# Kernel tuning notes

Hardware: AMD Instinct MI355X
Metric: run time of the kernel (lower is better)

The kernel has to match this reference:

```python
import jax, jax.numpy as jnp
import numpy as np

B, N = 2, 6
H, W = 64, 64            # BEV grid
FH, FW = 32, 88          # camera feature map
DIM, FEAT_DIM = 128, 128
HEADS, DH = 4, 32
QW1, QW2 = 8, 8          # query window
KW1, KW2 = 4, 11         # key/val window
IMG_H, IMG_W = 224, 480
EPS = 1e-5


def _ln(t, g, b):
    m = t.mean(-1, keepdims=True)
    v = ((t - m) ** 2).mean(-1, keepdims=True)
    return (t - m) / jnp.sqrt(v + EPS) * g + b


def _bn_relu_conv(t, g, b, Wc):
    # eval-mode BatchNorm2d (running_mean=0, running_var=1) -> ReLU -> 1x1 conv
    y = jax.nn.relu(t / jnp.sqrt(1.0 + EPS) * g[:, None, None] + b[:, None, None])
    return jnp.einsum('oc,nchw->nohw', Wc, y)


def _normalize(t, axis):
    n = jnp.sqrt(jnp.sum(t * t, axis=axis, keepdims=True))
    return t / jnp.maximum(n, 1e-12)


def _win(t, w1, w2):
    # (..., X*w1, Y*w2, d) -> (..., X, Y, w1, w2, d)
    s = t.shape
    t = t.reshape(*s[:-3], s[-3] // w1, w1, s[-2] // w2, w2, s[-1])
    return jnp.swapaxes(t, -4, -3)


def _unwin(t):
    # (..., X, Y, w1, w2, d) -> (..., X*w1, Y*w2, d)
    s = t.shape
    return jnp.swapaxes(t, -4, -3).reshape(*s[:-5], s[-5] * s[-3], s[-4] * s[-2], s[-1])


def _gridwin(t, w1, w2):
    bb, nn, Ht, Wt, d = t.shape
    t = t.reshape(bb, nn, w1, Ht // w1, w2, Wt // w2, d)
    return t.transpose(0, 1, 3, 5, 2, 4, 6)  # (b, n, X, Y, w1, w2, d)


def _cross_win_attn(qw, kw, vw, ln_g, ln_b, Wqkv, bqkv, Wp, bp, skip):
    b, n, X, Y, w1, w2, d = qw.shape
    f1, f2 = kw.shape[4], kw.shape[5]
    L = X * Y
    q = qw.transpose(0, 2, 3, 1, 4, 5, 6).reshape(b, L, n * w1 * w2, d)
    k = kw.transpose(0, 2, 3, 1, 4, 5, 6).reshape(b, L, n * f1 * f2, d)
    v = vw.transpose(0, 2, 3, 1, 4, 5, 6).reshape(b, L, n * f1 * f2, d)
    q = _ln(q, ln_g[0], ln_b[0]) @ Wqkv[0] + bqkv[0]
    k = _ln(k, ln_g[1], ln_b[1]) @ Wqkv[1] + bqkv[1]
    v = _ln(v, ln_g[2], ln_b[2]) @ Wqkv[2] + bqkv[2]
    split = lambda t: t.reshape(*t.shape[:-1], HEADS, DH)  # head-major channel split
    q, k, v = split(q), split(k), split(v)
    att = jax.nn.softmax(DH ** -0.5 * jnp.einsum('blqhd,blkhd->bhlqk', q, k), axis=-1)
    o = jnp.einsum('bhlqk,blkhd->blqhd', att, v).reshape(b, L, n * w1 * w2, HEADS * DH)
    o = o @ Wp + bp
    o = o.reshape(b, X, Y, n, w1, w2, d).mean(3)  # mean over cameras
    return o + skip


def _forward(x, grid, feature, I_inv, E_inv,
             bn_fl_g, bn_fl_b, W_fl, bn_fp_g, bn_fp_b, W_fp,
             W_bev, b_bev, W_img, W_cam,
             attn_ln_g, attn_ln_b, attn_Wqkv, attn_bqkv, attn_Wp, attn_bp,
             pn_g, pn_b, Wma, bma, Wmb, bmb, post_g, post_b):
    b, n = feature.shape[:2]
    # image plane (buffer)
    xs = jnp.linspace(0.0, 1.0, FW) * IMG_W
    ys = jnp.linspace(0.0, 1.0, FH) * IMG_H
    gx, gy = jnp.meshgrid(xs, ys)  # (FH, FW) each
    plane = jnp.stack([gx, gy, jnp.ones_like(gx)], 0).reshape(3, FH * FW)
    # camera embedding from translation column of E_inv
    c = E_inv[..., -1]                                   # (b, n, 4)
    c_embed = jnp.einsum('oc,bnc->bno', W_cam, c)        # (b, n, dim)
    # unprojected rays
    cam = jnp.einsum('bnij,jk->bnik', I_inv, plane)      # (b, n, 3, HW)
    cam = jnp.concatenate([cam, jnp.ones_like(cam[:, :, :1])], 2)
    d = jnp.einsum('bnij,bnjk->bnik', E_inv, cam)        # (b, n, 4, HW)
    d_img = d.reshape(b, n, 4, FH, FW)
    d_embed = jnp.einsum('oc,bnchw->bnohw', W_img, d_img)
    img_embed = _normalize(d_embed - c_embed[..., None, None], axis=2)
    # BEV positional embedding
    w_embed = jnp.einsum('oc,chw->ohw', W_bev, grid[:2]) + b_bev[:, None, None]
    bev_embed = _normalize(w_embed[None, None] - c_embed[..., None, None], axis=2)  # (b,n,dim,H,W)
    feat = feature.reshape(b * n, FEAT_DIM, FH, FW)
    key_im = img_embed + _bn_relu_conv(feat, bn_fp_g, bn_fp_b, W_fp).reshape(b, n, DIM, FH, FW)
    val_im = _bn_relu_conv(feat, bn_fl_g, bn_fl_b, W_fl).reshape(b, n, DIM, FH, FW)
    query = bev_embed + x[:, None]                       # (b, n, dim, H, W)
    # channel-last
    q_im = query.transpose(0, 1, 3, 4, 2)
    k_im = key_im.transpose(0, 1, 3, 4, 2)
    v_im = val_im.transpose(0, 1, 3, 4, 2)
    x_im = x.transpose(0, 2, 3, 1)
    # stage 1: local windows
    qw = _win(q_im, QW1, QW2)
    kw = _win(k_im, KW1, KW2)
    vw = _win(v_im, KW1, KW2)
    o1 = _cross_win_attn(qw, kw, vw, attn_ln_g[0], attn_ln_b[0], attn_Wqkv[0],
                         attn_bqkv[0], attn_Wp[0], attn_bp[0], _win(x_im, QW1, QW2))
    q1 = _unwin(o1)                                      # (b, H, W, d)
    q1 = q1 + jax.nn.gelu(_ln(q1, pn_g[0], pn_b[0]) @ Wma[0] + bma[0], approximate=False) @ Wmb[0] + bmb[0]
    # stage 2: grid (swapped) windows
    qg = jnp.broadcast_to(q1[:, None], (b, n) + q1.shape[1:])
    o2 = _cross_win_attn(_win(qg, QW1, QW2), _gridwin(k_im, KW1, KW2), _gridwin(v_im, KW1, KW2),
                         attn_ln_g[1], attn_ln_b[1], attn_Wqkv[1], attn_bqkv[1],
                         attn_Wp[1], attn_bp[1], _win(q1, QW1, QW2))
    q2 = _unwin(o2)
    q2 = q2 + jax.nn.gelu(_ln(q2, pn_g[1], pn_b[1]) @ Wma[1] + bma[1], approximate=False) @ Wmb[1] + bmb[1]
    out = _ln(q2, post_g, post_b)
    return out.transpose(0, 3, 1, 2)                     # (b, dim, H, W)


def setup_inputs() -> dict:
    key = jax.random.key(0)
    ks = jax.random.split(key, 16)
    rn = lambda i, shape, sc=0.02: jax.random.normal(ks[i], shape, dtype=jnp.float32) * sc
    return {
        'index': 0,
        'x': jax.random.normal(ks[0], (B, DIM, H, W), dtype=jnp.float32),
        'grid': jax.random.normal(ks[1], (2, H, W), dtype=jnp.float32),
        'feature': jax.random.normal(ks[2], (B, N, FEAT_DIM, FH, FW), dtype=jnp.float32),
        'I_inv': jax.random.normal(ks[3], (B, N, 3, 3), dtype=jnp.float32),
        'E_inv': jax.random.normal(ks[4], (B, N, 4, 4), dtype=jnp.float32),
        'bn_fl_g': jnp.ones((FEAT_DIM,), jnp.float32), 'bn_fl_b': jnp.zeros((FEAT_DIM,), jnp.float32),
        'W_fl': rn(5, (DIM, FEAT_DIM)),
        'bn_fp_g': jnp.ones((FEAT_DIM,), jnp.float32), 'bn_fp_b': jnp.zeros((FEAT_DIM,), jnp.float32),
        'W_fp': rn(6, (DIM, FEAT_DIM)),
        'W_bev': rn(7, (DIM, 2)), 'b_bev': jnp.zeros((DIM,), jnp.float32),
        'W_img': rn(8, (DIM, 4)), 'W_cam': rn(9, (DIM, 4)),
        'attn_ln_g': jnp.ones((2, 3, DIM), jnp.float32), 'attn_ln_b': jnp.zeros((2, 3, DIM), jnp.float32),
        'attn_Wqkv': rn(10, (2, 3, DIM, HEADS * DH)), 'attn_bqkv': jnp.zeros((2, 3, HEADS * DH), jnp.float32),
        'attn_Wp': rn(11, (2, HEADS * DH, DIM)), 'attn_bp': jnp.zeros((2, DIM), jnp.float32),
        'pn_g': jnp.ones((2, DIM), jnp.float32), 'pn_b': jnp.zeros((2, DIM), jnp.float32),
        'Wma': rn(12, (2, DIM, 2 * DIM)), 'bma': jnp.zeros((2, 2 * DIM), jnp.float32),
        'Wmb': rn(13, (2, 2 * DIM, DIM)), 'bmb': jnp.zeros((2, DIM), jnp.float32),
        'post_g': jnp.ones((DIM,), jnp.float32), 'post_b': jnp.zeros((DIM,), jnp.float32),
    }


def reference(index, x, grid, feature, I_inv, E_inv,
              bn_fl_g, bn_fl_b, W_fl, bn_fp_g, bn_fp_b, W_fp,
              W_bev, b_bev, W_img, W_cam,
              attn_ln_g, attn_ln_b, attn_Wqkv, attn_bqkv, attn_Wp, attn_bp,
              pn_g, pn_b, Wma, bma, Wmb, bmb, post_g, post_b):
    del index  # grid for this index is passed directly
    return _forward(x, grid, feature, I_inv, E_inv,
                    bn_fl_g, bn_fl_b, W_fl, bn_fp_g, bn_fp_b, W_fp,
                    W_bev, b_bev, W_img, W_cam,
                    attn_ln_g, attn_ln_b, attn_Wqkv, attn_bqkv, attn_Wp, attn_bp,
                    pn_g, pn_b, Wma, bma, Wmb, bmb, post_g, post_b)
```

## Files before the change

kernel.cpp:

```cpp
#include <hip/hip_runtime.h>
#include <math.h>


typedef __attribute__((ext_vector_type(8))) short short8;
typedef __attribute__((ext_vector_type(4))) float f32x4;

__device__ __forceinline__ unsigned short f2bf(float f){
  union { float f; unsigned u; } v; v.f = f;
  unsigned r = v.u + 0x7FFF + ((v.u >> 16) & 1);
  return (unsigned short)(r >> 16);
}
__device__ __forceinline__ float bf2f(unsigned short h){
  union { unsigned u; float f; } v; v.u = ((unsigned)h) << 16; return v.f;
}
__device__ __forceinline__ void store_bf16x8(unsigned short* p, const float* v){
  union { short8 s8; unsigned short u[8]; } u;
  #pragma unroll
  for (int i=0;i<8;i++) u.u[i] = f2bf(v[i]);
  *(short8*)p = u.s8;
}

__device__ __forceinline__ float gelu_erf(float x){
  float z = x * 0.70710678118654752f;
  float a = fabsf(z);
  float t = 1.0f / fmaf(0.3275911f, a, 1.0f);
  float p = t*(0.254829592f + t*(-0.284496736f + t*(1.421413741f +
            t*(-1.453152027f + t*1.061405429f))));
  float er = 1.0f - p*__expf(-a*a);
  er = copysignf(er, z);
  return 0.5f * x * (1.0f + er);
}

__device__ __forceinline__ size_t remap_kv(int tok, int mode){
  int bn = tok / 2816; int p = tok - bn*2816;
  int b = bn / 6, n = bn - b*6;
  int i = p / 88, j = p - i*88;
  int l, t;
  if (mode == 1){
    int jw = j / 11;
    l = (i >> 2)*8 + jw;
    t = n*44 + (i & 3)*11 + (j - jw*11);
  } else {
    l = (i & 7)*8 + (j & 7);
    t = n*44 + (i >> 3)*11 + (j >> 3);
  }
  return (size_t)((b*64 + l)*264 + t);
}

__global__ __launch_bounds__(256) void k_prepconv(
    const float* __restrict__ qkv, const float* __restrict__ wp,
    const float* __restrict__ wma, const float* __restrict__ wmb,
    unsigned short* __restrict__ Wt,
    const float* __restrict__ abqkv, float* __restrict__ biasP,
    const float* __restrict__ gridp, const float* __restrict__ Wbev,
    const float* __restrict__ bbev, const float* __restrict__ x,
    const float* __restrict__ lg, const float* __restrict__ lb,
    const float* __restrict__ Einv, const float* __restrict__ Wcam,
    unsigned short* __restrict__ QPh,
    const float* __restrict__ feat,
    const float* __restrict__ gfp, const float* __restrict__ bfp,
    const float* __restrict__ Wfp,
    const float* __restrict__ gfl, const float* __restrict__ bfl,
    const float* __restrict__ Wfl,
    const float* __restrict__ Iinv, const float* __restrict__ Wimg,
    unsigned short* __restrict__ KPh, unsigned short* __restrict__ KP2h,
    unsigned short* __restrict__ VPh, unsigned short* __restrict__ VP2h){
  constexpr int KP_ = 136;
  __shared__ unsigned short sW[128*KP_];
  __shared__ unsigned short sA[128*KP_];
  __shared__ __align__(16) float sMisc[2560];
  const int bid = blockIdx.x;
  const int tid = threadIdx.x;

  if (bid < 528){
    float* sg_  = sMisc;
    float* sb_  = sMisc + 128;
    float* sMean= sMisc + 256;
    float* sRstd= sMisc + 384;
    float* sRn  = sMisc + 512;
    float* sCE  = sMisc + 640;
    float4* sWI4= (float4*)(sMisc + 768);
    float* sIE  = sMisc + 1280;
    float* sB1  = sMisc + 1312;
    float* sB2  = sMisc + 1440;
    const int which = (bid >= 264);
    const int cbid = which ? bid - 264 : bid;
    const int m1 = which ? 2 : 1;
    const int m2 = which ? 5 : 4;
    const float* gg = which ? gfl : gfp;
    const float* bb = which ? bfl : bfp;
    const float* Wf = which ? Wfl : Wfp;
    unsigned short* Oa = which ? VPh : KPh;
    unsigned short* Ob = which ? VP2h : KP2h;
    const int base = cbid * 128;
    const int bn = base / 2816;
    const int pbase = base - bn*2816;
    if (tid < 128){ sg_[tid]=gg[tid]; sb_[tid]=bb[tid]; }
    if (!which){
      if (tid < 128){
        const float* E = Einv + bn*16;
        float4 wc = *(const float4*)(Wcam + tid*4);
        sCE[tid] = wc.x*E[3] + wc.y*E[7] + wc.z*E[11] + wc.w*E[15];
        sWI4[tid] = *(const float4*)(Wimg + tid*4);
      }
      if (tid < 25) sIE[tid] = (tid < 9) ? Iinv[bn*9 + tid] : Einv[bn*16 + (tid-9)];
    }
    for (int i = tid; i < 2048; i += 256){
      int n = i >> 4, k8 = (i & 15) << 3;
      const float* wsp = Wf + (size_t)n*128 + k8;
      float4 f0 = *(const float4*)wsp;
      float4 f1 = *(const float4*)(wsp+4);
      float v8[8] = {f0.x,f0.y,f0.z,f0.w,f1.x,f1.y,f1.z,f1.w};
      store_bf16x8(&sW[n*KP_ + k8], v8);
    }
    {
      int n = tid & 127, wsel = tid >> 7;
      int m = wsel ? m2 : m1;
      const float* W = qkv + m*16384;
      const float* lnb = lb + m*128;
      float s = abqkv[m*128 + n];
      for (int k=0;k<128;k++) s = fmaf(lnb[k], W[k*128 + n], s);
      (wsel ? sB2 : sB1)[n] = s;
    }
    const float RSQ = rsqrtf(1.0f + 1e-5f);
    {
      int prow = tid & 127, cseg = tid >> 7;
      int p = pbase + prow;
      const float* fb = feat + ((size_t)bn*128 + cseg*64)*2816 + p;
      #pragma unroll 8
      for (int i=0;i<64;i+=2){
        int c = cseg*64 + i;
        float t0 = fb[(size_t)i*2816] * RSQ;
        float t1 = fb[(size_t)(i+1)*2816] * RSQ;
        float y0 = fmaxf(fmaf(t0, sg_[c],   sb_[c]),   0.f);
        float y1 = fmaxf(fmaf(t1, sg_[c+1], sb_[c+1]), 0.f);
        unsigned u = (unsigned)f2bf(y0) | ((unsigned)f2bf(y1) << 16);
        *(unsigned*)&sA[prow*KP_ + c] = u;
      }
    }
    __syncthreads();
    const int lane = tid & 63, wv = tid >> 6;
    const int lane15 = lane & 15, quad = lane >> 4;
    const int n0 = wv * 32;
    const unsigned short* aptr = sA + lane15*KP_ + quad*8;
    const unsigned short* bptr = sW + (size_t)(n0 + lane15)*KP_ + quad*8;
    f32x4 acc[8][2];
    #pragma unroll
    for (int mt=0; mt<8; mt++){ acc[mt][0]=(f32x4)0.f; acc[mt][1]=(f32x4)0.f; }
    #pragma unroll
    for (int kk=0; kk<4; kk++){
      short8 af[8], bf2v[2];
      #pragma unroll
      for (int mt=0; mt<8; mt++) af[mt] = *(const short8*)(aptr + mt*16*KP_ + kk*32);
      bf2v[0] = *(const short8*)(bptr + kk*32);
      bf2v[1] = *(const short8*)(bptr + 16*KP_ + kk*32);
      #pragma unroll
      for (int mt=0; mt<8; mt++){
        acc[mt][0] = __builtin_amdgcn_mfma_f32_16x16x32_bf16(af[mt], bf2v[0], acc[mt][0], 0,0,0);
        acc[mt][1] = __builtin_amdgcn_mfma_f32_16x16x32_bf16(af[mt], bf2v[1], acc[mt][1], 0,0,0);
      }
    }
    __syncthreads();
    if (!which){
      const int r = tid >> 1, half = tid & 1;
      int p = pbase + r;
      int ii = p / 88, jj = p - ii*88;
      float xs = (float)jj * (480.0f/87.0f);
      float ys = (float)ii * (224.0f/31.0f);
      float c0 = sIE[0]*xs + sIE[1]*ys + sIE[2];
      float c1 = sIE[3]*xs + sIE[4]*ys + sIE[5];
      float c2 = sIE[6]*xs + sIE[7]*ys + sIE[8];
      float d0 = sIE[9]*c0  + sIE[10]*c1 + sIE[11]*c2 + sIE[12];
      float d1 = sIE[13]*c0 + sIE[14]*c1 + sIE[15]*c2 + sIE[16];
      float d2 = sIE[17]*c0 + sIE[18]*c1 + sIE[19]*c2 + sIE[20];
      float d3 = sIE[21]*c0 + sIE[22]*c1 + sIE[23]*c2 + sIE[24];
      float sq = 0.f;
      #pragma unroll 8
      for (int k=0;k<64;k++){
        int c = half*64 + k;
        float4 w = sWI4[c];
        float de = w.x*d0 + w.y*d1 + w.z*d2 + w.w*d3 - sCE[c];
        sA[r*KP_ + c] = f2bf(de);
        sq = fmaf(de, de, sq);
      }
      sq += __shfl_xor(sq, 1);
      if (half == 0) sRn[r] = 1.0f / fmaxf(sqrtf(sq), 1e-12f);
    }
    {
      const float* Wsrc = qkv + m1*16384;
      const float* gvv = lg + m1*128;
      for (int idx = tid; idx < 8192; idx += 256){
        int n = idx & 127, k2 = (idx >> 7) << 1;
        float v0 = Wsrc[(size_t)k2*128 + n]     * gvv[k2];
        float v1 = Wsrc[(size_t)(k2+1)*128 + n] * gvv[k2+1];
        *(unsigned*)&sW[n*KP_ + k2] = (unsigned)f2bf(v0) | ((unsigned)f2bf(v1) << 16);
      }
    }
    __syncthreads();
    #pragma unroll
    for (int mt=0; mt<8; mt++){
      #pragma unroll
      for (int nt=0; nt<2; nt++){
        int col = n0 + nt*16 + lane15;
        #pragma unroll
        for (int r4=0; r4<4; r4++){
          int row = mt*16 + quad*4 + r4;
          float v = acc[mt][nt][r4];
          if (!which) v += bf2f(sA[row*KP_ + col]) * sRn[row];
          sA[row*KP_ + col] = f2bf(v);
        }
      }
    }
    __syncthreads();
    {
      int r = tid >> 1, part = tid & 1;
      float s=0.f, s2=0.f;
      #pragma unroll 8
      for (int k=0;k<64;k++){
        float v = bf2f(sA[r*KP_ + part*64 + k]);
        s += v; s2 = fmaf(v,v,s2);
      }
      s += __shfl_xor(s, 1); s2 += __shfl_xor(s2, 1);
      if (part == 0){
        float mean = s*(1.f/128.f);
        sMean[r] = mean;
        sRstd[r] = rsqrtf(fmaxf(s2*(1.f/128.f) - mean*mean, 0.f) + 1e-5f);
      }
    }
    __syncthreads();
    for (int i = tid; i < 2048; i += 256){
      int row = i >> 4, seg = i & 15;
      float mean = sMean[row], rstd = sRstd[row];
      union { short8 s; unsigned short u[8]; } t;
      t.s = *(const short8*)&sA[row*KP_ + seg*8];
      float v[8];
      #pragma unroll
      for (int k=0;k<8;k++) v[k] = (bf2f(t.u[k]) - mean)*rstd;
      store_bf16x8(&sA[row*KP_ + seg*8], v);
    }
    __syncthreads();
    #pragma unroll
    for (int mt=0; mt<8; mt++){ acc[mt][0]=(f32x4)0.f; acc[mt][1]=(f32x4)0.f; }
    #pragma unroll
    for (int kk=0; kk<4; kk++){
      short8 af[8], bf2v[2];
      #pragma unroll
      for (int mt=0; mt<8; mt++) af[mt] = *(const short8*)(aptr + mt*16*KP_ + kk*32);
      bf2v[0] = *(const short8*)(bptr + kk*32);
      bf2v[1] = *(const short8*)(bptr + 16*KP_ + kk*32);
      #pragma unroll
      for (int mt=0; mt<8; mt++){
        acc[mt][0] = __builtin_amdgcn_mfma_f32_16x16x32_bf16(af[mt], bf2v[0], acc[mt][0], 0,0,0);
        acc[mt][1] = __builtin_amdgcn_mfma_f32_16x16x32_bf16(af[mt], bf2v[1], acc[mt][1], 0,0,0);
      }
    }
    __syncthreads();
    #pragma unroll
    for (int mt=0; mt<8; mt++){
      #pragma unroll
      for (int nt=0; nt<2; nt++){
        int col = n0 + nt*16 + lane15;
        float bsv = sB1[col];
        #pragma unroll
        for (int r4=0; r4<4; r4++){
          int row = mt*16 + quad*4 + r4;
          sW[row*KP_ + col] = f2bf(acc[mt][nt][r4] + bsv);
        }
      }
    }
    __syncthreads();
    for (int i = tid; i < 2048; i += 256){
      int row = i >> 4, seg = i & 15;
      size_t orow = remap_kv(base + row, 1);
      *(short8*)(Oa + orow*128 + seg*8) = *(const short8*)&sW[row*KP_ + seg*8];
    }
    __syncthreads();
    {
      const float* Wsrc = qkv + m2*16384;
      const float* gvv = lg + m2*128;
      for (int idx = tid; idx < 8192; idx += 256){
        int n = idx & 127, k2 = (idx >> 7) << 1;
        float v0 = Wsrc[(size_t)k2*128 + n]     * gvv[k2];
        float v1 = Wsrc[(size_t)(k2+1)*128 + n] * gvv[k2+1];
        *(unsigned*)&sW[n*KP_ + k2] = (unsigned)f2bf(v0) | ((unsigned)f2bf(v1) << 16);
      }
    }
    __syncthreads();
    #pragma unroll
    for (int mt=0; mt<8; mt++){ acc[mt][0]=(f32x4)0.f; acc[mt][1]=(f32x4)0.f; }
    #pragma unroll
    for (int kk=0; kk<4; kk++){
      short8 af[8], bf2v[2];
      #pragma unroll
      for (int mt=0; mt<8; mt++) af[mt] = *(const short8*)(aptr + mt*16*KP_ + kk*32);
      bf2v[0] = *(const short8*)(bptr + kk*32);
      bf2v[1] = *(const short8*)(bptr + 16*KP_ + kk*32);
      #pragma unroll
      for (int mt=0; mt<8; mt++){
        acc[mt][0] = __builtin_amdgcn_mfma_f32_16x16x32_bf16(af[mt], bf2v[0], acc[mt][0], 0,0,0);
        acc[mt][1] = __builtin_amdgcn_mfma_f32_16x16x32_bf16(af[mt], bf2v[1], acc[mt][1], 0,0,0);
      }
    }
    __syncthreads();
    #pragma unroll
    for (int mt=0; mt<8; mt++){
      #pragma unroll
      for (int nt=0; nt<2; nt++){
        int col = n0 + nt*16 + lane15;
        float bsv = sB2[col];
        #pragma unroll
        for (int r4=0; r4<4; r4++){
          int row = mt*16 + quad*4 + r4;
          sA[row*KP_ + col] = f2bf(acc[mt][nt][r4] + bsv);
        }
      }
    }
    __syncthreads();
    for (int i = tid; i < 2048; i += 256){
      int row = i >> 4, seg = i & 15;
      size_t orow = remap_kv(base + row, 2);
      *(short8*)(Ob + orow*128 + seg*8) = *(const short8*)&sA[row*KP_ + seg*8];
    }
  } else if (bid < 1040){
    const float QSCALE = 0.17677669529663687f;
    float* sx = sMisc;
    int* rowoff = (int*)(sMisc + 2176);
    int bid2 = bid - 528;
    int b = bid2 >> 8; int pp0 = (bid2 & 255) << 4;
    for (int idx = tid; idx < 8192; idx += 256){
      int n = idx & 127, k2 = (idx >> 7) << 1;
      float v0 = qkv[(size_t)k2*128 + n];
      float v1 = qkv[(size_t)(k2+1)*128 + n];
      *(unsigned*)&sW[n*KP_ + k2] = (unsigned)f2bf(v0) | ((unsigned)f2bf(v1) << 16);
    }
    {
      int cg = tid >> 4, px = tid & 15;
      #pragma unroll
      for (int i=0;i<8;i++){
        int c = cg + 16*i;
        sx[c*17 + px] = x[(size_t)b*524288 + (size_t)c*4096 + pp0 + px];
      }
    }
    if (tid < 16){
      int pix = pp0 + tid; int h = pix >> 6, w = pix & 63;
      int l = (h>>3)*8 + (w>>3); int tq = (h&7)*8 + (w&7);
      rowoff[tid] = (b*64 + l)*384 + tq;
    }
    __syncthreads();
    int xid = tid >> 4, part = tid & 15;
    int pix = pp0 + xid;
    float g0 = gridp[pix], g1 = gridp[4096 + pix];
    float we[8], xv[8];
    #pragma unroll
    for (int k=0;k<8;k++){
      int o = part*8 + k;
      we[k] = Wbev[o*2]*g0 + Wbev[o*2+1]*g1 + bbev[o];
      xv[k] = sx[(part*8+k)*17 + xid];
    }
    for (int n=0; n<6; n++){
      const float* E = Einv + (b*6+n)*16;
      float v[8]; float sq = 0.f;
      #pragma unroll
      for (int k=0;k<8;k++){
        int o = part*8 + k;
        const float* Wc = Wcam + o*4;
        float ce = Wc[0]*E[3] + Wc[1]*E[7] + Wc[2]*E[11] + Wc[3]*E[15];
        float vv = we[k] - ce;
        v[k] = vv; sq = fmaf(vv, vv, sq);
      }
      #pragma unroll
      for (int off=8; off>0; off>>=1) sq += __shfl_xor(sq, off, 16);
      float rn = 1.0f / fmaxf(sqrtf(sq), 1e-12f);
      float q[8]; float s=0.f, s2=0.f;
      #pragma unroll
      for (int k=0;k<8;k++){
        q[k] = fmaf(v[k], rn, xv[k]);
        s += q[k]; s2 = fmaf(q[k], q[k], s2);
      }
      #pragma unroll
      for (int off=8; off>0; off>>=1){ s += __shfl_xor(s, off, 16); s2 += __shfl_xor(s2, off, 16); }
      float mean = s*(1.f/128.f);
      float rstd = rsqrtf(fmaxf(s2*(1.f/128.f) - mean*mean, 0.f) + 1e-5f);
      float o8[8];
      #pragma unroll
      for (int k=0;k<8;k++){
        int c = part*8 + k;
        o8[k] = fmaf((q[k]-mean)*rstd, lg[c], lb[c]);
      }
      store_bf16x8(sA + (size_t)(n*16 + xid)*KP_ + part*8, o8);
    }
    __syncthreads();
    const int lane = tid & 63, wv = tid >> 6;
    const int lane15 = lane & 15, quad = lane >> 4;
    const int n0 = wv * 32;
    f32x4 acc[6][2];
    #pragma unroll
    for (int mt=0; mt<6; mt++){ acc[mt][0]=(f32x4)0.f; acc[mt][1]=(f32x4)0.f; }
    const unsigned short* aptr = sA + lane15*KP_ + quad*8;
    const unsigned short* bptr = sW + (size_t)(n0 + lane15)*KP_ + quad*8;
    #pragma unroll
    for (int kk=0; kk<4; kk++){
      short8 af[6], bf2v[2];
      #pragma unroll
      for (int mt=0; mt<6; mt++) af[mt] = *(const short8*)(aptr + mt*16*KP_ + kk*32);
      bf2v[0] = *(const short8*)(bptr + kk*32);
      bf2v[1] = *(const short8*)(bptr + 16*KP_ + kk*32);
      #pragma unroll
      for (int mt=0; mt<6; mt++){
        acc[mt][0] = __builtin_amdgcn_mfma_f32_16x16x32_bf16(af[mt], bf2v[0], acc[mt][0], 0,0,0);
        acc[mt][1] = __builtin_amdgcn_mfma_f32_16x16x32_bf16(af[mt], bf2v[1], acc[mt][1], 0,0,0);
      }
    }
    __syncthreads();
    #pragma unroll
    for (int nt=0; nt<2; nt++){
      int col = n0 + nt*16 + lane15;
      float bsv = abqkv[col];
      #pragma unroll
      for (int mt=0; mt<6; mt++){
        #pragma unroll
        for (int r4=0; r4<4; r4++){
          int row = mt*16 + quad*4 + r4;
          sA[row*KP_ + col] = f2bf((acc[mt][nt][r4] + bsv) * QSCALE);
        }
      }
    }
    __syncthreads();
    for (int i = tid; i < 1536; i += 256){
      int r = i >> 4, seg = i & 15;
      size_t grow = (size_t)rowoff[r & 15] + (r >> 4)*64;
      *(short8*)(QPh + grow*128 + seg*8) = *(const short8*)&sA[r*KP_ + seg*8];
    }
  } else if (bid < 1076){
    const int sel[9]  = {0, 1,1, 2,2, 3,3,3,3};
    const int soff[9] = {49152, 0,16384, 0,32768, 0,16384,32768,49152};
    const int doff[9] = {49152, 98304,114688, 131072,163840,
                         196608,212992,229376,245760};
    const int Ns[9]   = {128, 128,128, 256,256, 128,128,128,128};
    int bidw = bid - 1040;
    int sg = bidw >> 2, q = bidw & 3;
    const float* srcs[4] = {qkv, wp, wma, wmb};
    const float* src = srcs[sel[sg]] + soff[sg];
    unsigned short* dst = Wt + doff[sg];
    int K = 128, N = Ns[sg];
    int quarter = (K*N) >> 2;
    bool fold = (sg == 0);
    const float* gv = lg + 384;
    for (int idx = q*quarter + tid; idx < (q+1)*quarter; idx += 256){
      int n = idx / K, k = idx - n*K;
      float v = src[k*N + n];
      if (fold) v *= gv[k];
      dst[idx] = f2bf(v);
    }
  } else {
    if (tid < 128){
      int n = tid;
      const float* lnb = lb + 384;
      const float* W = qkv + 49152;
      float s = abqkv[384 + n];
      for (int k=0;k<128;k++) s = fmaf(lnb[k], W[k*128 + n], s);
      biasP[384 + n] = s;
    }
  }
}

__global__ __launch_bounds__(256) void k_tail(
    const unsigned short* __restrict__ AOh,
    const float* __restrict__ skipf, int skipmode,
    const unsigned short* __restrict__ WtP, const float* __restrict__ abp,
    const float* __restrict__ png, const float* __restrict__ pnb,
    const unsigned short* __restrict__ WtMAa, const unsigned short* __restrict__ WtMAb,
    const float* __restrict__ bma,
    const unsigned short* __restrict__ WtMBa, const unsigned short* __restrict__ WtMBb,
    const float* __restrict__ bmb,
    float* __restrict__ Q1out,
    const unsigned short* __restrict__ WtQ2, const float* __restrict__ q2bias,
    float q2scale, unsigned short* __restrict__ QPout,
    const float* __restrict__ postg, const float* __restrict__ postb,
    float* __restrict__ out){
  constexpr int KP_ = 136;
  __shared__ unsigned short sW[128*KP_];
  __shared__ unsigned short sX[16*KP_];
  __shared__ unsigned short sH1[16*KP_];
  __shared__ unsigned short sH2[16*KP_];
  __shared__ float sCUR[16*132];
  __shared__ float sbias[128];
  __shared__ float sg[128], sb2[128];
  __shared__ float sMean[16], sRstd[16];
  const int tid = threadIdx.x;
  const int base = blockIdx.x * 16;
  const int lane = tid & 63, wv = tid >> 6;
  const int lane15 = lane & 15, quad = lane >> 4;
  const int n0 = wv * 32;

  short8 wreg[8];
  auto stageLoad = [&](const unsigned short* Wp){
    #pragma unroll
    for (int i=0;i<8;i++){
      int idx = tid + i*256;
      int n = idx >> 4, k8 = (idx & 15) << 3;
      wreg[i] = *(const short8*)(Wp + (size_t)n*128 + k8);
    }
  };
  auto stageWrite = [&](){
    #pragma unroll
    for (int i=0;i<8;i++){
      int idx = tid + i*256;
      int n = idx >> 4, k8 = (idx & 15) << 3;
      *(short8*)&sW[n*KP_ + k8] = wreg[i];
    }
  };
  auto domfma = [&](const unsigned short* Asrc, f32x4 acc[2]){
    const unsigned short* aptr = Asrc + lane15*KP_ + quad*8;
    const unsigned short* bptr = sW + (size_t)(n0 + lane15)*KP_ + quad*8;
    #pragma unroll
    for (int kk=0; kk<4; kk++){
      short8 a0 = *(const short8*)(aptr + kk*32);
      short8 b0 = *(const short8*)(bptr + kk*32);
      short8 b1 = *(const short8*)(bptr + 16*KP_ + kk*32);
      acc[0] = __builtin_amdgcn_mfma_f32_16x16x32_bf16(a0,b0,acc[0],0,0,0);
      acc[1] = __builtin_amdgcn_mfma_f32_16x16x32_bf16(a0,b1,acc[1],0,0,0);
    }
  };

  stageLoad(WtP);
  {
    const int r = tid >> 4, part = tid & 15;
    *(short8*)(sX + r*KP_ + part*8) =
      *(const short8*)(AOh + (size_t)(base+r)*128 + part*8);
  }
  if (tid < 128){ sbias[tid] = abp[tid]; sg[tid] = png[tid]; sb2[tid] = pnb[tid]; }
  stageWrite();
  __syncthreads();
  stageLoad(WtMAa);
  {
    f32x4 acc[2];
    acc[0]=(f32x4)0.f; acc[1]=(f32x4)0.f;
    domfma(sX, acc);
    #pragma unroll
    for (int nt=0; nt<2; nt++){
      int col = n0 + nt*16 + lane15;
      float bsv = sbias[col];
      #pragma unroll
      for (int r4=0; r4<4; r4++){
        int row = quad*4 + r4;
        int rrow = base + row;
        float v = acc[nt][r4] + bsv;
        if (skipmode == 1){
          int bb = rrow >> 12, l = (rrow >> 6) & 63, pp = rrow & 63;
          int pix = (((l>>3)*8 + (pp>>3)) << 6) + (l&7)*8 + (pp&7);
          v += skipf[(size_t)bb*524288 + (size_t)col*4096 + pix];
        } else {
          v += skipf[(size_t)rrow*128 + col];
        }
        sCUR[row*132 + col] = v;
      }
    }
  }
  __syncthreads();
  stageWrite();
  if (tid < 128) sbias[tid] = bma[tid];
  {
    const int r = tid >> 4, part = tid & 15;
    float v[8];
    #pragma unroll
    for (int k=0;k<8;k++) v[k] = sCUR[r*132 + part*8 + k];
    float s=0.f, s2=0.f;
    #pragma unroll
    for (int k=0;k<8;k++){ s += v[k]; s2 = fmaf(v[k],v[k],s2); }
    #pragma unroll
    for (int off=8; off>0; off>>=1){ s += __shfl_xor(s, off, 16); s2 += __shfl_xor(s2, off, 16); }
    float mean = s*(1.f/128.f);
    float rstd = rsqrtf(fmaxf(s2*(1.f/128.f) - mean*mean, 0.f) + 1e-5f);
    #pragma unroll
    for (int k=0;k<8;k++){
      int c = part*8 + k;
      v[k] = fmaf((v[k]-mean)*rstd, sg[c], sb2[c]);
    }
    store_bf16x8(sX + r*KP_ + part*8, v);
  }
  __syncthreads();
  stageLoad(WtMAb);
  {
    f32x4 acc[2];
    acc[0]=(f32x4)0.f; acc[1]=(f32x4)0.f;
    domfma(sX, acc);
    #pragma unroll
    for (int nt=0; nt<2; nt++){
      int col = n0 + nt*16 + lane15;
      float bsv = sbias[col];
      #pragma unroll
      for (int r4=0; r4<4; r4++){
        int row = quad*4 + r4;
        sH1[row*KP_ + col] = f2bf(gelu_erf(acc[nt][r4] + bsv));
      }
    }
  }
  __syncthreads();
  stageWrite();
  if (tid < 128) sbias[tid] = bma[128 + tid];
  __syncthreads();
  stageLoad(WtMBa);
  {
    f32x4 acc[2];
    acc[0]=(f32x4)0.f; acc[1]=(f32x4)0.f;
    domfma(sX, acc);
    #pragma unroll
    for (int nt=0; nt<2; nt++){
      int col = n0 + nt*16 + lane15;
      float bsv = sbias[col];
      #pragma unroll
      for (int r4=0; r4<4; r4++){
        int row = quad*4 + r4;
        sH2[row*KP_ + col] = f2bf(gelu_erf(acc[nt][r4] + bsv));
      }
    }
  }
  __syncthreads();
  stageWrite();
  if (tid < 128) sbias[tid] = bmb[tid];
  __syncthreads();
  stageLoad(WtMBb);
  f32x4 acc[2];
  acc[0]=(f32x4)0.f; acc[1]=(f32x4)0.f;
  domfma(sH1, acc);
  __syncthreads();
  stageWrite();
  __syncthreads();
  if (WtQ2) stageLoad(WtQ2);
  domfma(sH2, acc);
  if (out == nullptr){
    #pragma unroll
    for (int nt=0; nt<2; nt++){
      int col = n0 + nt*16 + lane15;
      float bsv = sbias[col];
      #pragma unroll
      for (int r4=0; r4<4; r4++){
        int row = quad*4 + r4;
        float v = acc[nt][r4] + bsv + sCUR[row*132 + col];
        sCUR[row*132 + col] = v;
        Q1out[(size_t)(base+row)*128 + col] = v;
      }
    }
    __syncthreads();
    {
      const int r = tid >> 4, part = tid & 15;
      float s=0.f, s2=0.f;
      #pragma unroll
      for (int k=0;k<8;k++){
        float v = sCUR[r*132 + part*8 + k];
        s += v; s2 = fmaf(v,v,s2);
      }
      #pragma unroll
      for (int off=8; off>0; off>>=1){ s += __shfl_xor(s, off, 16); s2 += __shfl_xor(s2, off, 16); }
      if (part == 0){
        float mean = s*(1.f/128.f);
        sMean[r] = mean;
        sRstd[r] = rsqrtf(fmaxf(s2*(1.f/128.f) - mean*mean, 0.f) + 1e-5f);
      }
    }
    __syncthreads();
    {
      const int r = tid >> 4, part = tid & 15;
      float mean = sMean[r], rstd = sRstd[r];
      float v[8];
      #pragma unroll
      for (int k=0;k<8;k++) v[k] = (sCUR[r*132 + part*8 + k] - mean)*rstd;
      store_bf16x8(sX + r*KP_ + part*8, v);
    }
    stageWrite();
    if (tid < 128) sbias[tid] = q2bias[tid];
    __syncthreads();
    f32x4 a2[2];
    a2[0]=(f32x4)0.f; a2[1]=(f32x4)0.f;
    domfma(sX, a2);
    #pragma unroll
    for (int nt=0; nt<2; nt++){
      int col = n0 + nt*16 + lane15;
      float bsv = sbias[col];
      #pragma unroll
      for (int r4=0; r4<4; r4++){
        int row = quad*4 + r4;
        sH1[row*KP_ + col] = f2bf((a2[nt][r4] + bsv) * q2scale);
      }
    }
    __syncthreads();
    {
      int row = tid >> 4, seg = tid & 15;
      *(short8*)(QPout + (size_t)(base+row)*128 + seg*8) = *(const short8*)&sH1[row*KP_ + seg*8];
    }
  } else {
    float res[2][4];
    #pragma unroll
    for (int nt=0; nt<2; nt++){
      int col = n0 + nt*16 + lane15;
      float bsv = sbias[col];
      #pragma unroll
      for (int r4=0; r4<4; r4++){
        int row = quad*4 + r4;
        res[nt][r4] = acc[nt][r4] + bsv + sCUR[row*132 + col];
      }
    }
    __syncthreads();
    #pragma unroll
    for (int nt=0; nt<2; nt++){
      int col = n0 + nt*16 + lane15;
      #pragma unroll
      for (int r4=0; r4<4; r4++){
        int row = quad*4 + r4;
        sCUR[row*132 + col] = res[nt][r4];
      }
    }
    __syncthreads();
    {
      const int r = tid >> 4, part = tid & 15;
      float s=0.f, s2=0.f;
      #pragma unroll
      for (int k=0;k<8;k++){
        float v = sCUR[r*132 + part*8 + k];
        s += v; s2 = fmaf(v,v,s2);
      }
      #pragma unroll
      for (int off=8; off>0; off>>=1){ s += __shfl_xor(s, off, 16); s2 += __shfl_xor(s2, off, 16); }
      if (part == 0){
        float mean = s*(1.f/128.f);
        sMean[r] = mean;
        sRstd[r] = rsqrtf(fmaxf(s2*(1.f/128.f) - mean*mean, 0.f) + 1e-5f);
      }
    }
    __syncthreads();
    {
      int c = tid & 127, half = tid >> 7;
      int b = base >> 12, l = (base >> 6) & 63, p0 = base & 63;
      float go = postg[c], bo = postb[c];
      int p = p0 + half*8;
      int hrow = (l>>3)*8 + (p>>3);
      int w0 = (l&7)*8;
      float rr[8];
      #pragma unroll
      for (int j=0;j<8;j++){
        int row = half*8 + j;
        rr[j] = fmaf((sCUR[row*132 + c] - sMean[row])*sRstd[row], go, bo);
      }
      size_t obase = ((size_t)(b*128 + c))*4096 + (size_t)hrow*64 + w0;
      *(float4*)&out[obase]   = make_float4(rr[0],rr[1],rr[2],rr[3]);
      *(float4*)&out[obase+4] = make_float4(rr[4],rr[5],rr[6],rr[7]);
    }
  }
}

__global__ __launch_bounds__(256) void k_attn2(const unsigned short* __restrict__ QPh,
    const unsigned short* __restrict__ KPh, const unsigned short* __restrict__ VPh,
    unsigned short* __restrict__ AOh, int nrep, int nQ){
  __shared__ unsigned short Ksh[288*40];
  __shared__ unsigned short Vt[32*296];
  __shared__ unsigned short Psh[4*16*40];
  __shared__ float rs[4*16];
  int hd = blockIdx.x & 3; int bl = blockIdx.x >> 2;
  size_t kvbase = (size_t)bl*264;
  int tid = threadIdx.x;
  const int wv = tid >> 6, lane = tid & 63;
  const int lane15 = lane & 15, quad = lane >> 4;
  short8 qf_cur = *(const short8*)(QPh +
      (size_t)(bl*nQ + wv*16 + lane15)*128 + hd*32 + quad*8);
  for (int idx = tid; idx < 1056; idx += 256){
    int row = idx >> 2, seg = idx & 3;
    *(short8*)&Ksh[row*40 + seg*8] =
      *(const short8*)(KPh + (kvbase+row)*128 + hd*32 + seg*8);
  }
  for (int idx = tid; idx < 96; idx += 256){
    int row = 264 + (idx>>2), seg = idx & 3;
    short8 z = {0,0,0,0,0,0,0,0};
    *(short8*)&Ksh[row*40 + seg*8] = z;
  }
  for (int idx = tid; idx < 528; idx += 256){
    int kp = idx >> 2, seg = idx & 3;
    union { short8 s; unsigned short u[8]; } a, b;
    a.s = *(const short8*)(VPh + (kvbase + 2*kp)*128 + hd*32 + seg*8);
    b.s = *(const short8*)(VPh + (kvbase + 2*kp + 1)*128 + hd*32 + seg*8);
    #pragma unroll
    for (int i=0;i<8;i++)
      *(unsigned*)&Vt[(seg*8+i)*296 + 2*kp] = (unsigned)a.u[i] | ((unsigned)b.u[i] << 16);
  }
  for (int idx = tid; idx < 384; idx += 256){
    int d = idx / 12, kp = 264 + (idx % 12)*2;
    *(unsigned*)&Vt[d*296 + kp] = 0u;
  }
  __syncthreads();
  unsigned short* Pw = Psh + wv*640;
  float* rsw = rs + wv*16;
  short8 vfrag[9][2];
  #pragma unroll
  for (int kc=0; kc<9; kc++){
    vfrag[kc][0] = *(const short8*)&Vt[(lane15)*296      + kc*32 + quad*8];
    vfrag[kc][1] = *(const short8*)&Vt[(16+lane15)*296   + kc*32 + quad*8];
  }
  f32x4 macc0 = (f32x4)0.f, macc1 = (f32x4)0.f;
  for (int cam = 0; cam < nrep; cam++){
    short8 qf = qf_cur;
    if (cam + 1 < nrep){
      int qrown = bl*nQ + ((cam+1)*4 + wv)*16 + lane15;
      qf_cur = *(const short8*)(QPh + (size_t)qrown*128 + hd*32 + quad*8);
    }
    f32x4 oa0 = (f32x4)0.f, oa1 = (f32x4)0.f;
    float rsum = 0.f;
    #pragma unroll
    for (int kc=0; kc<9; kc++){
      #pragma unroll
      for (int sub=0; sub<2; sub++){
        int kt = kc*2 + sub;
        short8 kf = *(const short8*)&Ksh[(kt*16 + lane15)*40 + quad*8];
        f32x4 st = __builtin_amdgcn_mfma_f32_16x16x32_bf16(kf, qf, (f32x4)0.f, 0,0,0);
        int kbase = kt*16 + quad*4;
        float e0 = (kbase+0 < 264) ? __expf(st[0]) : 0.f;
        float e1 = (kbase+1 < 264) ? __expf(st[1]) : 0.f;
        float e2 = (kbase+2 < 264) ? __expf(st[2]) : 0.f;
        float e3 = (kbase+3 < 264) ? __expf(st[3]) : 0.f;
        rsum += (e0+e1)+(e2+e3);
        uint2 pk;
        pk.x = (unsigned)f2bf(e0) | ((unsigned)f2bf(e1) << 16);
        pk.y = (unsigned)f2bf(e2) | ((unsigned)f2bf(e3) << 16);
        *(uint2*)&Pw[lane15*40 + sub*16 + quad*4] = pk;
      }
      short8 pf = *(const short8*)&Pw[lane15*40 + quad*8];
      oa0 = __builtin_amdgcn_mfma_f32_16x16x32_bf16(pf, vfrag[kc][0], oa0, 0,0,0);
      oa1 = __builtin_amdgcn_mfma_f32_16x16x32_bf16(pf, vfrag[kc][1], oa1, 0,0,0);
    }
    rsum += __shfl_xor(rsum, 16);
    rsum += __shfl_xor(rsum, 32);
    if (lane < 16) rsw[lane] = rsum;
    f32x4 rv = *(f32x4*)&rsw[quad*4];
    #pragma unroll
    for (int r=0;r<4;r++){
      float inv = 1.f / rv[r];
      macc0[r] = fmaf(oa0[r], inv, macc0[r]);
      macc1[r] = fmaf(oa1[r], inv, macc1[r]);
    }
  }
  float sc = (nrep == 6) ? (1.f/6.f) : 1.f;
  int pixb = wv*16 + quad*4;
  #pragma unroll
  for (int r=0;r<4;r++){
    size_t rowo = ((size_t)(bl*64 + pixb + r))*128 + hd*32;
    AOh[rowo + lane15]      = f2bf(macc0[r]*sc);
    AOh[rowo + 16 + lane15] = f2bf(macc1[r]*sc);
  }
}

extern "C" void kernel_launch(void* const* d_in, const int* in_sizes, int n_in,
                              void* d_out, int out_size, void* d_ws, size_t ws_size,
                              hipStream_t stream) {
  (void)in_sizes; (void)n_in; (void)out_size; (void)ws_size;
  const float* x     = (const float*)d_in[1];
  const float* gridp = (const float*)d_in[2];
  const float* feat  = (const float*)d_in[3];
  const float* Iinv  = (const float*)d_in[4];
  const float* Einv  = (const float*)d_in[5];
  const float* gfl   = (const float*)d_in[6];
  const float* bfl   = (const float*)d_in[7];
  const float* Wfl   = (const float*)d_in[8];
  const float* gfp   = (const float*)d_in[9];
  const float* bfp   = (const float*)d_in[10];
  const float* Wfp   = (const float*)d_in[11];
  const float* Wbev  = (const float*)d_in[12];
  const float* bbev  = (const float*)d_in[13];
  const float* Wimg  = (const float*)d_in[14];
  const float* Wcam  = (const float*)d_in[15];
  const float* alng  = (const float*)d_in[16];
  const float* alnb  = (const float*)d_in[17];
  const float* aWqkv = (const float*)d_in[18];
  const float* abqkv = (const float*)d_in[19];
  const float* aWp   = (const float*)d_in[20];
  const float* abp   = (const float*)d_in[21];
  const float* png   = (const float*)d_in[22];
  const float* pnb   = (const float*)d_in[23];
  const float* Wma   = (const float*)d_in[24];
  const float* bma   = (const float*)d_in[25];
  const float* Wmb   = (const float*)d_in[26];
  const float* bmb   = (const float*)d_in[27];
  const float* postg = (const float*)d_in[28];
  const float* postb = (const float*)d_in[29];
  float* out = (float*)d_out;
  float* ws  = (float*)d_ws;
  const float QSC = 0.17677669529663687f;

  float* biasP = ws;
  unsigned short* Wt   = (unsigned short*)(ws + 2048);
  unsigned short* K1h  = (unsigned short*)(ws + 149504);
  unsigned short* V1h  = K1h + 4325376;
  unsigned short* KPh  = V1h + 4325376;
  unsigned short* VPh  = KPh + 4325376;
  unsigned short* KP2h = VPh + 4325376;
  unsigned short* VP2h = KP2h + 4325376;
  unsigned short* QPh  = VP2h + 4325376;
  unsigned short* Qbh  = QPh + 6291456;
  unsigned short* AOh  = Qbh + 6291456;
  float* Q1f = (float*)(AOh + 1048576);

  unsigned short* WtQ2 = Wt + 49152;
  unsigned short* WtP1 = Wt + 98304;    unsigned short* WtP2 = Wt + 114688;
  unsigned short* WtMA1 = Wt + 131072;  unsigned short* WtMA2 = Wt + 163840;
  unsigned short* WtMB1a = Wt + 196608; unsigned short* WtMB1b = Wt + 212992;
  unsigned short* WtMB2a = Wt + 229376; unsigned short* WtMB2b = Wt + 245760;

  k_prepconv<<<1077, 256, 0, stream>>>(aWqkv, aWp, Wma, Wmb, Wt,
      abqkv, biasP, gridp, Wbev, bbev, x, alng, alnb, Einv, Wcam, QPh,
      feat, gfp, bfp, Wfp, gfl, bfl, Wfl, Iinv, Wimg,
      KPh, KP2h, VPh, VP2h);

  k_attn2<<<512, 256, 0, stream>>>(QPh, KPh, VPh, AOh, 6, 384);
  k_tail<<<512, 256, 0, stream>>>(AOh, x, 1, WtP1, abp, png, pnb,
      WtMA1, WtMA1+16384, bma, WtMB1a, WtMB1b, bmb, Q1f,
      WtQ2, biasP+384, QSC, QPh,
      nullptr, nullptr, nullptr);
  k_attn2<<<512, 256, 0, stream>>>(QPh, KP2h, VP2h, AOh, 1, 64);
  k_tail<<<512, 256, 0, stream>>>(AOh, Q1f, 3, WtP2, abp+128, png+128, pnb+128,
      WtMA2, WtMA2+16384, bma+256, WtMB2a, WtMB2b, bmb+128, nullptr,
      nullptr, nullptr, 0.f, nullptr,
      postg, postb, out);
}
```

Baseline: 240.9 us.

## Split attention work across eight waves with shared-memory reduction

Doubles the attention block to 512 threads. In the six-camera pass each half of the block handles three cameras, and in the single-camera pass each half handles a separate range of key chunks. Partial outputs and row sums are combined through shared memory before the final write. This aims to shorten the serial per-wave loop and raise parallelism on a grid of only 512 blocks, at the cost of extra syncs, a reduction step and lower occupancy headroom from the 512-thread launch bound. In the key-split pass each half normalises with the combined row sum, which is valid because no max subtraction is used.

```diff
diff --git a/kernel.cpp b/kernel.cpp
--- a/kernel.cpp
+++ b/kernel.cpp
@@ -749,31 +749,55 @@
   }
 }
 
-__global__ __launch_bounds__(256) void k_attn2(const unsigned short* __restrict__ QPh,
+#define KC_BODY(kcv) { \
+  _Pragma("unroll") \
+  for (int sub=0; sub<2; sub++){ \
+    int kt = (kcv)*2 + sub; \
+    short8 kf = *(const short8*)&Ksh[(kt*16 + lane15)*40 + quad*8]; \
+    f32x4 st = __builtin_amdgcn_mfma_f32_16x16x32_bf16(kf, qf, (f32x4)0.f, 0,0,0); \
+    int kbase = kt*16 + quad*4; \
+    float e0 = (kbase+0 < 264) ? __expf(st[0]) : 0.f; \
+    float e1 = (kbase+1 < 264) ? __expf(st[1]) : 0.f; \
+    float e2 = (kbase+2 < 264) ? __expf(st[2]) : 0.f; \
+    float e3 = (kbase+3 < 264) ? __expf(st[3]) : 0.f; \
+    rsum += (e0+e1)+(e2+e3); \
+    uint2 pk; \
+    pk.x = (unsigned)f2bf(e0) | ((unsigned)f2bf(e1) << 16); \
+    pk.y = (unsigned)f2bf(e2) | ((unsigned)f2bf(e3) << 16); \
+    *(uint2*)&Pw[lane15*40 + sub*16 + quad*4] = pk; \
+  } \
+  short8 pf = *(const short8*)&Pw[lane15*40 + quad*8]; \
+  oa0 = __builtin_amdgcn_mfma_f32_16x16x32_bf16(pf, vfrag[kcv][0], oa0, 0,0,0); \
+  oa1 = __builtin_amdgcn_mfma_f32_16x16x32_bf16(pf, vfrag[kcv][1], oa1, 0,0,0); \
+}
+
+__global__ __launch_bounds__(512) void k_attn2(const unsigned short* __restrict__ QPh,
     const unsigned short* __restrict__ KPh, const unsigned short* __restrict__ VPh,
     unsigned short* __restrict__ AOh, int nrep, int nQ){
   __shared__ unsigned short Ksh[288*40];
   __shared__ unsigned short Vt[32*296];
-  __shared__ unsigned short Psh[4*16*40];
-  __shared__ float rs[4*16];
+  __shared__ unsigned short Psh[8*16*40];
+  __shared__ float rs[8*16];
   int hd = blockIdx.x & 3; int bl = blockIdx.x >> 2;
   size_t kvbase = (size_t)bl*264;
   int tid = threadIdx.x;
   const int wv = tid >> 6, lane = tid & 63;
+  const int qw = wv & 3, ch = wv >> 2;
   const int lane15 = lane & 15, quad = lane >> 4;
+  const int cam_first = (nrep == 6) ? ch*3 : 0;
   short8 qf_cur = *(const short8*)(QPh +
-      (size_t)(bl*nQ + wv*16 + lane15)*128 + hd*32 + quad*8);
-  for (int idx = tid; idx < 1056; idx += 256){
+      (size_t)(bl*nQ + (cam_first*4 + qw)*16 + lane15)*128 + hd*32 + quad*8);
+  for (int idx = tid; idx < 1056; idx += 512){
     int row = idx >> 2, seg = idx & 3;
     *(short8*)&Ksh[row*40 + seg*8] =
       *(const short8*)(KPh + (kvbase+row)*128 + hd*32 + seg*8);
   }
-  for (int idx = tid; idx < 96; idx += 256){
+  for (int idx = tid; idx < 96; idx += 512){
     int row = 264 + (idx>>2), seg = idx & 3;
     short8 z = {0,0,0,0,0,0,0,0};
     *(short8*)&Ksh[row*40 + seg*8] = z;
   }
-  for (int idx = tid; idx < 528; idx += 256){
+  for (int idx = tid; idx < 528; idx += 512){
     int kp = idx >> 2, seg = idx & 3;
     union { short8 s; unsigned short u[8]; } a, b;
     a.s = *(const short8*)(VPh + (kvbase + 2*kp)*128 + hd*32 + seg*8);
@@ -782,7 +806,7 @@
     for (int i=0;i<8;i++)
       *(unsigned*)&Vt[(seg*8+i)*296 + 2*kp] = (unsigned)a.u[i] | ((unsigned)b.u[i] << 16);
   }
-  for (int idx = tid; idx < 384; idx += 256){
+  for (int idx = tid; idx < 384; idx += 512){
     int d = idx / 12, kp = 264 + (idx % 12)*2;
     *(unsigned*)&Vt[d*296 + kp] = 0u;
   }
@@ -795,55 +819,83 @@
     vfrag[kc][0] = *(const short8*)&Vt[(lane15)*296      + kc*32 + quad*8];
     vfrag[kc][1] = *(const short8*)&Vt[(16+lane15)*296   + kc*32 + quad*8];
   }
-  f32x4 macc0 = (f32x4)0.f, macc1 = (f32x4)0.f;
-  for (int cam = 0; cam < nrep; cam++){
+  float* red = (float*)Psh;
+  if (nrep == 6){
+    f32x4 macc0 = (f32x4)0.f, macc1 = (f32x4)0.f;
+    #pragma unroll
+    for (int ci = 0; ci < 3; ci++){
+      int cam = ch*3 + ci;
+      short8 qf = qf_cur;
+      if (ci + 1 < 3){
+        int qrown = bl*nQ + ((cam+1)*4 + qw)*16 + lane15;
+        qf_cur = *(const short8*)(QPh + (size_t)qrown*128 + hd*32 + quad*8);
+      }
+      f32x4 oa0 = (f32x4)0.f, oa1 = (f32x4)0.f;
+      float rsum = 0.f;
+      #pragma unroll
+      for (int kc=0; kc<9; kc++) KC_BODY(kc)
+      rsum += __shfl_xor(rsum, 16);
+      rsum += __shfl_xor(rsum, 32);
+      if (lane < 16) rsw[lane] = rsum;
+      f32x4 rv = *(f32x4*)&rsw[quad*4];
+      #pragma unroll
+      for (int r=0;r<4;r++){
+        float inv = 1.f / rv[r];
+        macc0[r] = fmaf(oa0[r], inv, macc0[r]);
+        macc1[r] = fmaf(oa1[r], inv, macc1[r]);
+      }
+    }
+    __syncthreads();
+    if (ch == 1){
+      float* dst = red + (size_t)(qw*64 + lane)*8;
+      #pragma unroll
+      for (int r=0;r<4;r++){ dst[r] = macc0[r]; dst[4+r] = macc1[r]; }
+    }
+    __syncthreads();
+    if (ch == 0){
+      const float* src = red + (size_t)(qw*64 + lane)*8;
+      int pixb = qw*16 + quad*4;
+      #pragma unroll
+      for (int r=0;r<4;r++){
+        size_t rowo = ((size_t)(bl*64 + pixb + r))*128 + hd*32;
+        AOh[rowo + lane15]      = f2bf((macc0[r] + src[r])   * (1.f/6.f));
+        AOh[rowo + 16 + lane15] = f2bf((macc1[r] + src[4+r]) * (1.f/6.f));
+      }
+    }
+  } else {
     short8 qf = qf_cur;
-    if (cam + 1 < nrep){
-      int qrown = bl*nQ + ((cam+1)*4 + wv)*16 + lane15;
-      qf_cur = *(const short8*)(QPh + (size_t)qrown*128 + hd*32 + quad*8);
-    }
     f32x4 oa0 = (f32x4)0.f, oa1 = (f32x4)0.f;
     float rsum = 0.f;
-    #pragma unroll
-    for (int kc=0; kc<9; kc++){
-      #pragma unroll
-      for (int sub=0; sub<2; sub++){
-        int kt = kc*2 + sub;
-        short8 kf = *(const short8*)&Ksh[(kt*16 + lane15)*40 + quad*8];
-        f32x4 st = __builtin_amdgcn_mfma_f32_16x16x32_bf16(kf, qf, (f32x4)0.f, 0,0,0);
-        int kbase = kt*16 + quad*4;
-        float e0 = (kbase+0 < 264) ? __expf(st[0]) : 0.f;
-        float e1 = (kbase+1 < 264) ? __expf(st[1]) : 0.f;
-        float e2 = (kbase+2 < 264) ? __expf(st[2]) : 0.f;
-        float e3 = (kbase+3 < 264) ? __expf(st[3]) : 0.f;
-        rsum += (e0+e1)+(e2+e3);
-        uint2 pk;
-        pk.x = (unsigned)f2bf(e0) | ((unsigned)f2bf(e1) << 16);
-        pk.y = (unsigned)f2bf(e2) | ((unsigned)f2bf(e3) << 16);
-        *(uint2*)&Pw[lane15*40 + sub*16 + quad*4] = pk;
-      }
-      short8 pf = *(const short8*)&Pw[lane15*40 + quad*8];
-      oa0 = __builtin_amdgcn_mfma_f32_16x16x32_bf16(pf, vfrag[kc][0], oa0, 0,0,0);
-      oa1 = __builtin_amdgcn_mfma_f32_16x16x32_bf16(pf, vfrag[kc][1], oa1, 0,0,0);
+    if (ch == 0){
+      #pragma unroll
+      for (int kc=0; kc<5; kc++) KC_BODY(kc)
+    } else {
+      #pragma unroll
+      for (int kc=5; kc<9; kc++) KC_BODY(kc)
     }
     rsum += __shfl_xor(rsum, 16);
     rsum += __shfl_xor(rsum, 32);
     if (lane < 16) rsw[lane] = rsum;
-    f32x4 rv = *(f32x4*)&rsw[quad*4];
-    #pragma unroll
-    for (int r=0;r<4;r++){
-      float inv = 1.f / rv[r];
-      macc0[r] = fmaf(oa0[r], inv, macc0[r]);
-      macc1[r] = fmaf(oa1[r], inv, macc1[r]);
-    }
-  }
-  float sc = (nrep == 6) ? (1.f/6.f) : 1.f;
-  int pixb = wv*16 + quad*4;
-  #pragma unroll
-  for (int r=0;r<4;r++){
-    size_t rowo = ((size_t)(bl*64 + pixb + r))*128 + hd*32;
-    AOh[rowo + lane15]      = f2bf(macc0[r]*sc);
-    AOh[rowo + 16 + lane15] = f2bf(macc1[r]*sc);
+    __syncthreads();
+    if (ch == 1){
+      float* dst = red + (size_t)(qw*64 + lane)*8;
+      #pragma unroll
+      for (int r=0;r<4;r++){ dst[r] = oa0[r]; dst[4+r] = oa1[r]; }
+    }
+    __syncthreads();
+    if (ch == 0){
+      const float* src = red + (size_t)(qw*64 + lane)*8;
+      f32x4 rv0 = *(f32x4*)&rs[qw*16 + quad*4];
+      f32x4 rv1 = *(f32x4*)&rs[(4+qw)*16 + quad*4];
+      int pixb = qw*16 + quad*4;
+      #pragma unroll
+      for (int r=0;r<4;r++){
+        float inv = 1.f / (rv0[r] + rv1[r]);
+        size_t rowo = ((size_t)(bl*64 + pixb + r))*128 + hd*32;
+        AOh[rowo + lane15]      = f2bf((oa0[r] + src[r])   * inv);
+        AOh[rowo + 16 + lane15] = f2bf((oa1[r] + src[4+r]) * inv);
+      }
+    }
   }
 }
 
@@ -908,12 +960,12 @@
       feat, gfp, bfp, Wfp, gfl, bfl, Wfl, Iinv, Wimg,
       KPh, KP2h, VPh, VP2h);
 
-  k_attn2<<<512, 256, 0, stream>>>(QPh, KPh, VPh, AOh, 6, 384);
+  k_attn2<<<512, 512, 0, stream>>>(QPh, KPh, VPh, AOh, 6, 384);
   k_tail<<<512, 256, 0, stream>>>(AOh, x, 1, WtP1, abp, png, pnb,
       WtMA1, WtMA1+16384, bma, WtMB1a, WtMB1b, bmb, Q1f,
       WtQ2, biasP+384, QSC, QPh,
       nullptr, nullptr, nullptr);
-  k_attn2<<<512, 256, 0, stream>>>(QPh, KP2h, VP2h, AOh, 1, 64);
+  k_attn2<<<512, 512, 0, stream>>>(QPh, KP2h, VP2h, AOh, 1, 64);
   k_tail<<<512, 256, 0, stream>>>(AOh, Q1f, 3, WtP2, abp+128, png+128, pnb+128,
       WtMA2, WtMA2+16384, bma+256, WtMB2a, WtMB2b, bmb+128, nullptr,
       nullptr, nullptr, 0.f, nullptr,
```

Result: no change. 240.1 us, median of 2 (-0.3%).
